# Kernel tuning notes

Measured on AMD Instinct MI355X. Metric: run time of the kernel, lower is better.

Reference implementation:

```python
import jax, jax.numpy as jnp
import numpy as np

B, IN, H, M = 65536, 128, 256, 32


def setup_inputs() -> dict:
    key = jax.random.key(0)
    ks = jax.random.split(key, 8)
    s_i = 1.0 / np.sqrt(IN + H)
    s_m = 1.0 / np.sqrt(M)
    return {
        "input": jax.random.normal(ks[0], (B, IN), jnp.float32),
        "media": jax.random.normal(ks[1], (B, M), jnp.float32),
        "h_t": jax.random.normal(ks[2], (B, H), jnp.float32),
        "c_t": jax.random.normal(ks[3], (B, H), jnp.float32),
        "Wi": jax.random.normal(ks[4], (H, IN + H), jnp.float32) * s_i,
        "bi": jax.random.normal(ks[5], (H,), jnp.float32) * s_i,
        "Wm": jax.random.normal(ks[6], (H, M), jnp.float32) * s_m,
        "bm": jax.random.normal(ks[7], (H,), jnp.float32) * s_m,
    }


def reference(input, media, h_t, c_t, Wi, bi, Wm, bm):
    # original, so all gates share one pre-activation g.
    combined = jnp.concatenate([input, h_t], axis=1)
    g = combined @ Wi.T + bi                     # [B, H]
    gate = jax.nn.sigmoid(g)                     # i == f == o
    c = c_t * gate + jnp.tanh(g) * gate          # new cell state
    c_r = jnp.tanh(c)
    m = jax.nn.sigmoid(media @ Wm.T + bm)        # media gate [B, H]
    c_f = c - c_r + c_r * m
    h = jnp.tanh(c_f) * gate
    # classification=False -> output is h; returns (output, h, c)
    return (h, h, c)
```

## Files before the change

kernel.cpp:

```cpp
#include <hip/hip_runtime.h>

#define BB  65536
#define INW 128
#define HH  256
#define MM  32
#define KK  (INW + HH)

typedef __attribute__((ext_vector_type(8))) short bf16x8;
typedef __attribute__((ext_vector_type(4))) float f32x4;

__device__ __forceinline__ unsigned f32_to_bf16(float f) {
    union { float f; unsigned u; } v; v.f = f;
    return (v.u + 0x7fffu + ((v.u >> 16) & 1u)) >> 16;
}

__device__ __forceinline__ bf16x8 cvt8(float4 a, float4 b) {
    bf16x8 r;
    r[0] = (short)f32_to_bf16(a.x); r[1] = (short)f32_to_bf16(a.y);
    r[2] = (short)f32_to_bf16(a.z); r[3] = (short)f32_to_bf16(a.w);
    r[4] = (short)f32_to_bf16(b.x); r[5] = (short)f32_to_bf16(b.y);
    r[6] = (short)f32_to_bf16(b.z); r[7] = (short)f32_to_bf16(b.w);
    return r;
}

__device__ __forceinline__ float rcp_f(float x) { return __builtin_amdgcn_rcpf(x); }
__device__ __forceinline__ float sigmoid_f(float x) { return rcp_f(1.0f + __expf(-x)); }
__device__ __forceinline__ float tanh_f(float x) { return 1.0f - 2.0f * rcp_f(__expf(2.0f * x) + 1.0f); }

__global__ void cvt_weights(const float* __restrict__ Wi, const float* __restrict__ Wm,
                            unsigned short* __restrict__ Wi_bf, unsigned short* __restrict__ Wm_bf) {
    int i = blockIdx.x * 256 + threadIdx.x;
    if (i < HH * KK) Wi_bf[i] = (unsigned short)f32_to_bf16(Wi[i]);
    if (i < HH * MM) Wm_bf[i] = (unsigned short)f32_to_bf16(Wm[i]);
}

__global__ __launch_bounds__(256) void rlstm_main(
    const float* __restrict__ input, const float* __restrict__ media,
    const float* __restrict__ h_t,   const float* __restrict__ c_t,
    const unsigned short* __restrict__ Wi_bf, const float* __restrict__ bi,
    const unsigned short* __restrict__ Wm_bf, const float* __restrict__ bm,
    float* __restrict__ out)
{
    const int tid  = threadIdx.x;
    const int wave = tid >> 6;
    const int lane = tid & 63;
    const int lrow = lane & 15;
    const int quad = lane >> 4;

    const int m0 = blockIdx.x * 32 + (wave >> 1) * 16;
    const int n0 = (wave & 1) * 128;

    f32x4 accg[8], accm[8];
#pragma unroll
    for (int t = 0; t < 8; ++t) {
        accg[t] = (f32x4){0.f, 0.f, 0.f, 0.f};
        accm[t] = (f32x4){0.f, 0.f, 0.f, 0.f};
    }

    const int arow = m0 + lrow;

    {
        const float4* ap = (const float4*)(media + (size_t)arow * MM + quad * 8);
        float4 a0 = ap[0], a1 = ap[1];
        bf16x8 af = cvt8(a0, a1);
        const unsigned short* wb = Wm_bf + (size_t)(n0 + lrow) * MM + quad * 8;
#pragma unroll
        for (int t = 0; t < 8; ++t) {
            bf16x8 bf = *(const bf16x8*)(wb + t * 16 * MM);
            accm[t] = __builtin_amdgcn_mfma_f32_16x16x32_bf16(af, bf, accm[t], 0, 0, 0);
        }
    }

    {
        const unsigned short* wbase = Wi_bf + (size_t)(n0 + lrow) * KK + quad * 8;
#pragma unroll
        for (int kc = 0; kc < 4; ++kc) {
            const float* src = input + (size_t)arow * INW + kc * 32 + quad * 8;
            float4 a0 = ((const float4*)src)[0];
            float4 a1 = ((const float4*)src)[1];
            bf16x8 af = cvt8(a0, a1);
            const unsigned short* wb = wbase + kc * 32;
#pragma unroll
            for (int t = 0; t < 8; ++t) {
                bf16x8 bf = *(const bf16x8*)(wb + t * 16 * KK);
                accg[t] = __builtin_amdgcn_mfma_f32_16x16x32_bf16(af, bf, accg[t], 0, 0, 0);
            }
        }
#pragma unroll
        for (int kc = 4; kc < 12; ++kc) {
            const float* src = h_t + (size_t)arow * HH + (kc - 4) * 32 + quad * 8;
            float4 a0 = ((const float4*)src)[0];
            float4 a1 = ((const float4*)src)[1];
            bf16x8 af = cvt8(a0, a1);
            const unsigned short* wb = wbase + kc * 32;
#pragma unroll
            for (int t = 0; t < 8; ++t) {
                bf16x8 bf = *(const bf16x8*)(wb + t * 16 * KK);
                accg[t] = __builtin_amdgcn_mfma_f32_16x16x32_bf16(af, bf, accg[t], 0, 0, 0);
            }
        }
    }

    const size_t outH = (size_t)BB * HH;
#pragma unroll
    for (int t = 0; t < 8; ++t) {
        const int col = n0 + t * 16 + lrow;
        const float bi_v = bi[col];
        const float bm_v = bm[col];
#pragma unroll
        for (int r = 0; r < 4; ++r) {
            const int row = m0 + quad * 4 + r;
            const size_t idx = (size_t)row * HH + col;
            float g    = accg[t][r] + bi_v;
            float mp   = accm[t][r] + bm_v;
            float gate = sigmoid_f(g);
            float tg   = tanh_f(g);
            float ct   = c_t[idx];
            float c    = ct * gate + tg * gate;
            float cr   = tanh_f(c);
            float mg   = sigmoid_f(mp);
            float cf   = c - cr + cr * mg;
            float h    = tanh_f(cf) * gate;
            out[idx]            = h;
            out[idx + outH]     = h;
            out[idx + 2 * outH] = c;
        }
    }
}

extern "C" void kernel_launch(void* const* d_in, const int* in_sizes, int n_in,
                              void* d_out, int out_size, void* d_ws, size_t ws_size,
                              hipStream_t stream) {
    const float* input = (const float*)d_in[0];
    const float* media = (const float*)d_in[1];
    const float* h_t   = (const float*)d_in[2];
    const float* c_t   = (const float*)d_in[3];
    const float* Wi    = (const float*)d_in[4];
    const float* bi    = (const float*)d_in[5];
    const float* Wm    = (const float*)d_in[6];
    const float* bm    = (const float*)d_in[7];
    float* out = (float*)d_out;

    unsigned short* Wi_bf = (unsigned short*)d_ws;
    unsigned short* Wm_bf = Wi_bf + HH * KK;

    hipLaunchKernelGGL(cvt_weights, dim3((HH * KK + 255) / 256), dim3(256), 0, stream,
                       Wi, Wm, Wi_bf, Wm_bf);
    hipLaunchKernelGGL(rlstm_main, dim3(BB / 32), dim3(256), 0, stream,
                       input, media, h_t, c_t, Wi_bf, bi, Wm_bf, bm, out);
}
```

Measured before the change: 420.1 us.

## Pre-pack weights in MFMA fragment order and swap operands for vectorized epilogue

The weight conversion kernel now writes bf16 weights in per-lane MFMA fragment order, so each lane loads contiguous 16-byte chunks instead of strided rows. The MFMA operands are swapped (weights as A, activations as B), so each lane's accumulator holds four consecutive columns of one row. That lets c_t, bias loads and the three output stores become float4 vector accesses instead of scalar strided ones. The media GEMM is also moved into the epilogue to cut live accumulator registers.

After: 391.7 us. 1.07x faster.

```diff
diff --git a/kernel.cpp b/kernel.cpp
--- a/kernel.cpp
+++ b/kernel.cpp
@@ -5,21 +5,22 @@
 #define HH  256
 #define MM  32
 #define KK  (INW + HH)
+#define NKC 12
 
 typedef __attribute__((ext_vector_type(8))) short bf16x8;
 typedef __attribute__((ext_vector_type(4))) float f32x4;
 
-__device__ __forceinline__ unsigned f32_to_bf16(float f) {
+__device__ __forceinline__ unsigned short f32_to_bf16(float f) {
     union { float f; unsigned u; } v; v.f = f;
-    return (v.u + 0x7fffu + ((v.u >> 16) & 1u)) >> 16;
+    return (unsigned short)((v.u + 0x7fffu + ((v.u >> 16) & 1u)) >> 16);
 }
 
-__device__ __forceinline__ bf16x8 cvt8(float4 a, float4 b) {
+__device__ __forceinline__ bf16x8 cvt8(f32x4 a, f32x4 b) {
     bf16x8 r;
-    r[0] = (short)f32_to_bf16(a.x); r[1] = (short)f32_to_bf16(a.y);
-    r[2] = (short)f32_to_bf16(a.z); r[3] = (short)f32_to_bf16(a.w);
-    r[4] = (short)f32_to_bf16(b.x); r[5] = (short)f32_to_bf16(b.y);
-    r[6] = (short)f32_to_bf16(b.z); r[7] = (short)f32_to_bf16(b.w);
+    r[0] = (short)f32_to_bf16(a[0]); r[1] = (short)f32_to_bf16(a[1]);
+    r[2] = (short)f32_to_bf16(a[2]); r[3] = (short)f32_to_bf16(a[3]);
+    r[4] = (short)f32_to_bf16(b[0]); r[5] = (short)f32_to_bf16(b[1]);
+    r[6] = (short)f32_to_bf16(b[2]); r[7] = (short)f32_to_bf16(b[3]);
     return r;
 }
 
@@ -27,18 +28,39 @@
 __device__ __forceinline__ float sigmoid_f(float x) { return rcp_f(1.0f + __expf(-x)); }
 __device__ __forceinline__ float tanh_f(float x) { return 1.0f - 2.0f * rcp_f(__expf(2.0f * x) + 1.0f); }
 
-__global__ void cvt_weights(const float* __restrict__ Wi, const float* __restrict__ Wm,
-                            unsigned short* __restrict__ Wi_bf, unsigned short* __restrict__ Wm_bf) {
-    int i = blockIdx.x * 256 + threadIdx.x;
-    if (i < HH * KK) Wi_bf[i] = (unsigned short)f32_to_bf16(Wi[i]);
-    if (i < HH * MM) Wm_bf[i] = (unsigned short)f32_to_bf16(Wm[i]);
+__global__ void pack_weights(const float* __restrict__ Wi, const float* __restrict__ Wm,
+                             unsigned short* __restrict__ Wi_p, unsigned short* __restrict__ Wm_p) {
+    int id = blockIdx.x * 256 + threadIdx.x;
+    if (id < 2 * NKC * 8 * 512) {
+        int blk = id >> 9;
+        int e   = id & 511;
+        int lane = e >> 3, j = e & 7;
+        int lrow = lane & 15, quad = lane >> 4;
+        int h  = blk / (NKC * 8);
+        int b  = blk % (NKC * 8);
+        int kc = b >> 3;
+        int t  = b & 7;
+        int n  = h * 128 + t * 16 + lrow;
+        int k  = kc * 32 + quad * 8 + j;
+        Wi_p[id] = f32_to_bf16(Wi[(size_t)n * KK + k]);
+    }
+    if (id < 2 * 8 * 512) {
+        int blk = id >> 9;
+        int e   = id & 511;
+        int lane = e >> 3, j = e & 7;
+        int lrow = lane & 15, quad = lane >> 4;
+        int h = blk >> 3;
+        int t = blk & 7;
+        int n = h * 128 + t * 16 + lrow;
+        Wm_p[id] = f32_to_bf16(Wm[(size_t)n * MM + quad * 8 + j]);
+    }
 }
 
 __global__ __launch_bounds__(256) void rlstm_main(
     const float* __restrict__ input, const float* __restrict__ media,
     const float* __restrict__ h_t,   const float* __restrict__ c_t,
-    const unsigned short* __restrict__ Wi_bf, const float* __restrict__ bi,
-    const unsigned short* __restrict__ Wm_bf, const float* __restrict__ bm,
+    const unsigned short* __restrict__ Wi_p, const float* __restrict__ bi,
+    const unsigned short* __restrict__ Wm_p, const float* __restrict__ bm,
     float* __restrict__ out)
 {
     const int tid  = threadIdx.x;
@@ -47,84 +69,70 @@
     const int lrow = lane & 15;
     const int quad = lane >> 4;
 
-    const int m0 = blockIdx.x * 32 + (wave >> 1) * 16;
-    const int n0 = (wave & 1) * 128;
+    const int m0   = blockIdx.x * 32 + (wave >> 1) * 16;
+    const int half = wave & 1;
+    const int n0   = half * 128;
 
-    f32x4 accg[8], accm[8];
-#pragma unroll
-    for (int t = 0; t < 8; ++t) {
-        accg[t] = (f32x4){0.f, 0.f, 0.f, 0.f};
-        accm[t] = (f32x4){0.f, 0.f, 0.f, 0.f};
-    }
+    const unsigned short* wip = Wi_p + (size_t)half * (NKC * 8 * 512);
+    const unsigned short* wmp = Wm_p + (size_t)half * (8 * 512);
 
     const int arow = m0 + lrow;
 
-    {
-        const float4* ap = (const float4*)(media + (size_t)arow * MM + quad * 8);
-        float4 a0 = ap[0], a1 = ap[1];
-        bf16x8 af = cvt8(a0, a1);
-        const unsigned short* wb = Wm_bf + (size_t)(n0 + lrow) * MM + quad * 8;
+    f32x4 md0 = *(const f32x4*)(media + (size_t)arow * MM + quad * 8);
+    f32x4 md1 = *(const f32x4*)(media + (size_t)arow * MM + quad * 8 + 4);
+
+    f32x4 accg[8];
+#pragma unroll
+    for (int t = 0; t < 8; ++t) accg[t] = (f32x4){0.f, 0.f, 0.f, 0.f};
+
+#pragma unroll
+    for (int kc = 0; kc < NKC; ++kc) {
+        const float* src = (kc < 4)
+            ? (input + (size_t)arow * INW + kc * 32 + quad * 8)
+            : (h_t   + (size_t)arow * HH  + (kc - 4) * 32 + quad * 8);
+        f32x4 a0 = ((const f32x4*)src)[0];
+        f32x4 a1 = ((const f32x4*)src)[1];
+        bf16x8 xf = cvt8(a0, a1);
+        const unsigned short* wb = wip + (size_t)kc * (8 * 512) + lane * 8;
 #pragma unroll
         for (int t = 0; t < 8; ++t) {
-            bf16x8 bf = *(const bf16x8*)(wb + t * 16 * MM);
-            accm[t] = __builtin_amdgcn_mfma_f32_16x16x32_bf16(af, bf, accm[t], 0, 0, 0);
+            bf16x8 wf = *(const bf16x8*)(wb + t * 512);
+            accg[t] = __builtin_amdgcn_mfma_f32_16x16x32_bf16(wf, xf, accg[t], 0, 0, 0);
         }
     }
 
-    {
-        const unsigned short* wbase = Wi_bf + (size_t)(n0 + lrow) * KK + quad * 8;
-#pragma unroll
-        for (int kc = 0; kc < 4; ++kc) {
-            const float* src = input + (size_t)arow * INW + kc * 32 + quad * 8;
-            float4 a0 = ((const float4*)src)[0];
-            float4 a1 = ((const float4*)src)[1];
-            bf16x8 af = cvt8(a0, a1);
-            const unsigned short* wb = wbase + kc * 32;
-#pragma unroll
-            for (int t = 0; t < 8; ++t) {
-                bf16x8 bf = *(const bf16x8*)(wb + t * 16 * KK);
-                accg[t] = __builtin_amdgcn_mfma_f32_16x16x32_bf16(af, bf, accg[t], 0, 0, 0);
-            }
-        }
-#pragma unroll
-        for (int kc = 4; kc < 12; ++kc) {
-            const float* src = h_t + (size_t)arow * HH + (kc - 4) * 32 + quad * 8;
-            float4 a0 = ((const float4*)src)[0];
-            float4 a1 = ((const float4*)src)[1];
-            bf16x8 af = cvt8(a0, a1);
-            const unsigned short* wb = wbase + kc * 32;
-#pragma unroll
-            for (int t = 0; t < 8; ++t) {
-                bf16x8 bf = *(const bf16x8*)(wb + t * 16 * KK);
-                accg[t] = __builtin_amdgcn_mfma_f32_16x16x32_bf16(af, bf, accg[t], 0, 0, 0);
-            }
-        }
-    }
-
+    bf16x8 mf = cvt8(md0, md1);
     const size_t outH = (size_t)BB * HH;
+    const size_t rowbase = (size_t)arow * HH;
 #pragma unroll
     for (int t = 0; t < 8; ++t) {
-        const int col = n0 + t * 16 + lrow;
-        const float bi_v = bi[col];
-        const float bm_v = bm[col];
+        bf16x8 wmf = *(const bf16x8*)(wmp + t * 512 + lane * 8);
+        f32x4 am = __builtin_amdgcn_mfma_f32_16x16x32_bf16(
+            wmf, mf, (f32x4){0.f, 0.f, 0.f, 0.f}, 0, 0, 0);
+
+        const int nb = n0 + t * 16 + quad * 4;
+        f32x4 bi4 = *(const f32x4*)(bi + nb);
+        f32x4 bm4 = *(const f32x4*)(bm + nb);
+        const size_t idx = rowbase + nb;
+        f32x4 ct4 = *(const f32x4*)(c_t + idx);
+
+        f32x4 h4, c4;
 #pragma unroll
         for (int r = 0; r < 4; ++r) {
-            const int row = m0 + quad * 4 + r;
-            const size_t idx = (size_t)row * HH + col;
-            float g    = accg[t][r] + bi_v;
-            float mp   = accm[t][r] + bm_v;
+            float g    = accg[t][r] + bi4[r];
+            float mp   = am[r] + bm4[r];
             float gate = sigmoid_f(g);
             float tg   = tanh_f(g);
-            float ct   = c_t[idx];
-            float c    = ct * gate + tg * gate;
+            float c    = ct4[r] * gate + tg * gate;
             float cr   = tanh_f(c);
             float mg   = sigmoid_f(mp);
             float cf   = c - cr + cr * mg;
             float h    = tanh_f(cf) * gate;
-            out[idx]            = h;
-            out[idx + outH]     = h;
-            out[idx + 2 * outH] = c;
+            h4[r] = h; c4[r] = c;
         }
+        *(f32x4*)(out + idx)            = h4;
+        *(f32x4*)(out + idx + outH)     = h4;
+        *(f32x4*)(out + idx + 2 * outH) = c4;
     }
 }
 
@@ -141,11 +149,11 @@
     const float* bm    = (const float*)d_in[7];
     float* out = (float*)d_out;
 
-    unsigned short* Wi_bf = (unsigned short*)d_ws;
-    unsigned short* Wm_bf = Wi_bf + HH * KK;
+    unsigned short* Wi_p = (unsigned short*)d_ws;
+    unsigned short* Wm_p = Wi_p + 2 * NKC * 8 * 512;
 
-    hipLaunchKernelGGL(cvt_weights, dim3((HH * KK + 255) / 256), dim3(256), 0, stream,
-                       Wi, Wm, Wi_bf, Wm_bf);
+    hipLaunchKernelGGL(pack_weights, dim3((2 * NKC * 8 * 512 + 255) / 256), dim3(256), 0, stream,
+                       Wi, Wm, Wi_p, Wm_p);
     hipLaunchKernelGGL(rlstm_main, dim3(BB / 32), dim3(256), 0, stream,
-                       input, media, h_t, c_t, Wi_bf, bi, Wm_bf, bm, out);
+                       input, media, h_t, c_t, Wi_p, bi, Wm_p, bm, out);
 }
```
